# Kernel optimization log

Hardware: AMD Instinct MI355X
Metric: run time of the kernel (lower is better)

## Reference

```python
import jax, jax.numpy as jnp
import numpy as np

B, L, E, DC, N = 1024, 64, 1024, 768, 16384
EPS = 1e-08


def setup_inputs() -> dict:
    key = jax.random.key(0)
    k1, k2, k3, k4, k5, k6 = jax.random.split(key, 6)
    inputs = jax.random.normal(k1, (B, 1, E), dtype=jnp.float32)
    text_emb = jax.random.normal(k2, (B, L, DC), dtype=jnp.float32)
    # padding mask: True = padded; valid lengths in [10, 60) so every row triggers the insert branch
    lengths = jax.random.randint(k3, (B,), 10, 60)
    attn_mask = jnp.arange(L)[None, :] >= lengths[:, None]
    proj_w = jax.random.normal(k4, (DC, E), dtype=jnp.float32) * 0.02
    proj_b = jnp.zeros((DC,), dtype=jnp.float32)
    codebook = jax.random.normal(k5, (N, DC), dtype=jnp.float32) * 0.02
    return {"inputs": inputs, "text_emb": text_emb, "attn_mask": attn_mask,
            "proj_w": proj_w, "proj_b": proj_b, "codebook": codebook}


def _soft_match(x, W):
    # x: [B, S, D], W: [N, D] -> soft codebook readout [B, S, D]
    xn = x / jnp.maximum(jnp.linalg.norm(x, axis=-1, keepdims=True), EPS)
    Wn = W / jnp.maximum(jnp.linalg.norm(W, axis=-1, keepdims=True), EPS)
    d = 1.0 - jnp.einsum('bsd,nd->bsn', xn, Wn)   # 1 - cosine similarity
    p = jax.nn.softmax(d, axis=-1)                 # softmax over codebook entries
    return jnp.einsum('bsn,nd->bsd', p, W)


def reference(inputs, text_emb, attn_mask, proj_w, proj_b, codebook):
    # proj: torch Linear -> x @ W.T + b
    x = jnp.einsum('bse,de->bsd', inputs, proj_w) + proj_b
    clue = _soft_match(x, codebook)                # [B, 1, DC]

    b, l = attn_mask.shape
    vl = l - jnp.sum(attn_mask, axis=1)            # valid length per row, [B]
    do = vl < 64                                   # insert only if there is room
    pos = jnp.arange(l)
    at_vl = pos[None, :] == vl[:, None]            # position valid_length
    at_prev = pos[None, :] == (vl - 1)[:, None]    # position valid_length-1
    prev_vec = text_emb[jnp.arange(b), jnp.clip(vl - 1, 0, l - 1)]  # [B, DC]

    sel_vl = (do[:, None] & at_vl)[..., None]
    sel_prev = (do[:, None] & at_prev)[..., None]
    new_text_emb = jnp.where(sel_vl, prev_vec[:, None, :], text_emb)
    new_text_emb = jnp.where(sel_prev, clue[:, 0, :][:, None, :], new_text_emb)
    new_attn_mask = attn_mask & ~(do[:, None] & at_vl)
    return new_text_emb, new_attn_mask, jnp.float32(0.0)
```

## Files before the change

### kernel.cpp

```cpp
#include <hip/hip_runtime.h>
#include <hip/hip_bf16.h>

#define B_  1024
#define L_  64
#define E_  1024
#define DC_ 768
#define N_  16384

typedef short bf16x8 __attribute__((ext_vector_type(8)));
typedef float f32x4  __attribute__((ext_vector_type(4)));


__global__ void detect_mask(const unsigned int* __restrict__ mi, int* __restrict__ flag) {
    __shared__ int notInt, notFlt;
    if (threadIdx.x == 0) { notInt = 0; notFlt = 0; }
    __syncthreads();
    int ni = 0, nf = 0;
    for (int i = threadIdx.x; i < 16384; i += 256) {
        unsigned v = mi[i];
        if (v > 1u) ni = 1;
        if (v != 0u && v != 0x3f800000u) nf = 1;
    }
    if (ni) notInt = 1;
    if (nf) notFlt = 1;
    __syncthreads();
    if (threadIdx.x == 0) *flag = (!notInt) ? 1 : ((!notFlt) ? 2 : 0);
}

__global__ void compute_vl(const void* __restrict__ mask, const int* __restrict__ flag,
                           int* __restrict__ vl) {
    int b = blockIdx.x * blockDim.x + threadIdx.x;
    if (b >= B_) return;
    int f = *flag;
    int s = 0;
    if (f == 1) {
        const int* m = (const int*)mask;
        for (int j = 0; j < L_; ++j) s += m[b * L_ + j];
    } else if (f == 2) {
        const float* m = (const float*)mask;
        for (int j = 0; j < L_; ++j) s += (m[b * L_ + j] != 0.0f) ? 1 : 0;
    } else {
        const unsigned char* m = (const unsigned char*)mask;
        for (int j = 0; j < L_; ++j) s += m[b * L_ + j];
    }
    vl[b] = L_ - s;
}

__global__ __launch_bounds__(256) void rownorm(const float* __restrict__ M,
                                               float* __restrict__ r, int cols) {
    int row = blockIdx.x;
    const float* p = M + (size_t)row * cols;
    float s = 0.0f;
    for (int c = threadIdx.x; c < cols; c += 256) { float v = p[c]; s += v * v; }
    for (int off = 32; off > 0; off >>= 1) s += __shfl_down(s, off);
    __shared__ float sm[4];
    if ((threadIdx.x & 63) == 0) sm[threadIdx.x >> 6] = s;
    __syncthreads();
    if (threadIdx.x == 0) {
        float t = sm[0] + sm[1] + sm[2] + sm[3];
        r[row] = 1.0f / fmaxf(sqrtf(t), 1e-8f);
    }
}

__global__ __launch_bounds__(256) void rownorm_bf16(const __hip_bfloat16* __restrict__ M,
                                                    float* __restrict__ r, int cols) {
    int row = blockIdx.x;
    const __hip_bfloat16* p = M + (size_t)row * cols;
    float s = 0.0f;
    for (int c = threadIdx.x; c < cols; c += 256) { float v = __bfloat162float(p[c]); s += v * v; }
    for (int off = 32; off > 0; off >>= 1) s += __shfl_down(s, off);
    __shared__ float sm[4];
    if ((threadIdx.x & 63) == 0) sm[threadIdx.x >> 6] = s;
    __syncthreads();
    if (threadIdx.x == 0) {
        float t = sm[0] + sm[1] + sm[2] + sm[3];
        r[row] = 1.0f / fmaxf(sqrtf(t), 1e-8f);
    }
}

__global__ __launch_bounds__(256) void prep_cb(const float* __restrict__ CB,
                                               __hip_bfloat16* __restrict__ CBb,
                                               __hip_bfloat16* __restrict__ CBt) {
    __shared__ float t[64][65];
    int n0 = blockIdx.x * 64, d0 = blockIdx.y * 64;
    int tid = threadIdx.x;
    #pragma unroll
    for (int i = 0; i < 16; ++i) {
        int r = (tid >> 6) + i * 4, c = tid & 63;
        float v = CB[(size_t)(n0 + r) * DC_ + d0 + c];
        t[r][c] = v;
        CBb[(size_t)(n0 + r) * DC_ + d0 + c] = __float2bfloat16(v);
    }
    __syncthreads();
    #pragma unroll
    for (int i = 0; i < 16; ++i) {
        int r = (tid >> 6) + i * 4, c = tid & 63;
        CBt[(size_t)(d0 + r) * N_ + n0 + c] = __float2bfloat16(t[c][r]);
    }
}

__global__ __launch_bounds__(256) void proj_gemm(const float* __restrict__ A,
                                                 const float* __restrict__ W,
                                                 const float* __restrict__ bias,
                                                 __hip_bfloat16* __restrict__ Xb) {
    __shared__ float As[64][17];
    __shared__ float Bs[64][17];
    int t = threadIdx.x;
    int tx = t & 15, ty = t >> 4;
    int m0 = blockIdx.y * 64, n0 = blockIdx.x * 64;
    float acc[4][4] = {};
    for (int k0 = 0; k0 < E_; k0 += 16) {
        #pragma unroll
        for (int i = 0; i < 4; ++i) {
            int r = (t >> 4) + i * 16, c = t & 15;
            As[r][c] = A[(size_t)(m0 + r) * E_ + k0 + c];
            Bs[r][c] = W[(size_t)(n0 + r) * E_ + k0 + c];
        }
        __syncthreads();
        #pragma unroll
        for (int k = 0; k < 16; ++k) {
            float a[4], b[4];
            #pragma unroll
            for (int i = 0; i < 4; ++i) a[i] = As[ty * 4 + i][k];
            #pragma unroll
            for (int j = 0; j < 4; ++j) b[j] = Bs[tx * 4 + j][k];
            #pragma unroll
            for (int i = 0; i < 4; ++i)
                #pragma unroll
                for (int j = 0; j < 4; ++j) acc[i][j] += a[i] * b[j];
        }
        __syncthreads();
    }
    #pragma unroll
    for (int i = 0; i < 4; ++i)
        #pragma unroll
        for (int j = 0; j < 4; ++j) {
            int m = m0 + ty * 4 + i, n = n0 + tx * 4 + j;
            Xb[(size_t)m * DC_ + n] = __float2bfloat16(acc[i][j] + bias[n]);
        }
}

__device__ __forceinline__ void stage_tile(const __hip_bfloat16* __restrict__ src, size_t ldk,
                                           __hip_bfloat16* smem, int wave, int lane) {
    #pragma unroll
    for (int s = 0; s < 2; ++s) {
        const int chunk = wave * 32 + s * 16;
        const int r = chunk + (lane >> 2);
        const int gslot = (lane & 3) ^ ((lane >> 2) & 3);
        const __hip_bfloat16* g = src + (size_t)r * ldk + gslot * 8;
        __builtin_amdgcn_global_load_lds(
            (const __attribute__((address_space(1))) void*)g,
            (__attribute__((address_space(3))) void*)(smem + chunk * 32), 16, 0, 0);
    }
}

__device__ __forceinline__ bf16x8 read_frag(const __hip_bfloat16* smem, int base_row, int lane) {
    const int r = base_row + (lane & 15);
    const int slot = ((lane >> 4) ^ r) & 3;
    return *(const bf16x8*)(smem + r * 32 + slot * 8);
}

__global__ __launch_bounds__(256) void score_mfma(const __hip_bfloat16* __restrict__ Xb,
                                                  const __hip_bfloat16* __restrict__ CBb,
                                                  const float* __restrict__ rX,
                                                  const float* __restrict__ rW,
                                                  __hip_bfloat16* __restrict__ P,
                                                  float* __restrict__ Z) {
    __shared__ __align__(16) __hip_bfloat16 As[128 * 32];
    __shared__ __align__(16) __hip_bfloat16 Bs[128 * 32];
    const int t = threadIdx.x, lane = t & 63, wave = t >> 6;
    const int wr = wave >> 1, wc = wave & 1;
    const int m0 = blockIdx.y * 128, n0 = blockIdx.x * 128;

    f32x4 acc[4][4];
    #pragma unroll
    for (int i = 0; i < 4; ++i)
        #pragma unroll
        for (int j = 0; j < 4; ++j) acc[i][j] = (f32x4){0.f, 0.f, 0.f, 0.f};

    const __hip_bfloat16* Asrc = Xb  + (size_t)m0 * DC_;
    const __hip_bfloat16* Bsrc = CBb + (size_t)n0 * DC_;
    for (int k0 = 0; k0 < DC_; k0 += 32) {
        stage_tile(Asrc + k0, DC_, As, wave, lane);
        stage_tile(Bsrc + k0, DC_, Bs, wave, lane);
        __syncthreads();
        bf16x8 af[4], bg[4];
        #pragma unroll
        for (int i = 0; i < 4; ++i) af[i] = read_frag(As, wr * 64 + i * 16, lane);
        #pragma unroll
        for (int j = 0; j < 4; ++j) bg[j] = read_frag(Bs, wc * 64 + j * 16, lane);
        #pragma unroll
        for (int i = 0; i < 4; ++i)
            #pragma unroll
            for (int j = 0; j < 4; ++j)
                acc[i][j] = __builtin_amdgcn_mfma_f32_16x16x32_bf16(af[i], bg[j], acc[i][j], 0, 0, 0);
        __syncthreads();
    }

    const int fr = lane & 15, fq = lane >> 4;
    float rw[4];
    #pragma unroll
    for (int j = 0; j < 4; ++j) rw[j] = rW[n0 + wc * 64 + j * 16 + fr];
    #pragma unroll
    for (int i = 0; i < 4; ++i) {
        const int mb = m0 + wr * 64 + i * 16 + fq * 4;
        float rx[4];
        #pragma unroll
        for (int q = 0; q < 4; ++q) rx[q] = rX[mb + q];
        float rs[4] = {0.f, 0.f, 0.f, 0.f};
        #pragma unroll
        for (int j = 0; j < 4; ++j) {
            const int n = n0 + wc * 64 + j * 16 + fr;
            #pragma unroll
            for (int q = 0; q < 4; ++q) {
                float e = __expf(-acc[i][j][q] * rx[q] * rw[j]);
                P[(size_t)(mb + q) * N_ + n] = __float2bfloat16(e);
                rs[q] += e;
            }
        }
        #pragma unroll
        for (int q = 0; q < 4; ++q) {
            float s = rs[q];
            s += __shfl_xor(s, 1); s += __shfl_xor(s, 2);
            s += __shfl_xor(s, 4); s += __shfl_xor(s, 8);
            if (fr == 0) atomicAdd(&Z[mb + q], s);
        }
    }
}

__global__ __launch_bounds__(256) void out_mfma(const __hip_bfloat16* __restrict__ P,
                                                const __hip_bfloat16* __restrict__ CBt,
                                                float* __restrict__ clue) {
    __shared__ __align__(16) __hip_bfloat16 As[128 * 32];
    __shared__ __align__(16) __hip_bfloat16 Bs[128 * 32];
    const int t = threadIdx.x, lane = t & 63, wave = t >> 6;
    const int wr = wave >> 1, wc = wave & 1;
    const int m0 = blockIdx.y * 128, d0 = blockIdx.x * 128;
    const int kbeg = blockIdx.z * (N_ / 8);

    f32x4 acc[4][4];
    #pragma unroll
    for (int i = 0; i < 4; ++i)
        #pragma unroll
        for (int j = 0; j < 4; ++j) acc[i][j] = (f32x4){0.f, 0.f, 0.f, 0.f};

    const __hip_bfloat16* Asrc = P   + (size_t)m0 * N_;
    const __hip_bfloat16* Bsrc = CBt + (size_t)d0 * N_;
    for (int kk = 0; kk < N_ / 8; kk += 32) {
        const int k0 = kbeg + kk;
        stage_tile(Asrc + k0, N_, As, wave, lane);
        stage_tile(Bsrc + k0, N_, Bs, wave, lane);
        __syncthreads();
        bf16x8 af[4], bg[4];
        #pragma unroll
        for (int i = 0; i < 4; ++i) af[i] = read_frag(As, wr * 64 + i * 16, lane);
        #pragma unroll
        for (int j = 0; j < 4; ++j) bg[j] = read_frag(Bs, wc * 64 + j * 16, lane);
        #pragma unroll
        for (int i = 0; i < 4; ++i)
            #pragma unroll
            for (int j = 0; j < 4; ++j)
                acc[i][j] = __builtin_amdgcn_mfma_f32_16x16x32_bf16(af[i], bg[j], acc[i][j], 0, 0, 0);
        __syncthreads();
    }

    const int fr = lane & 15, fq = lane >> 4;
    #pragma unroll
    for (int i = 0; i < 4; ++i) {
        const int mb = m0 + wr * 64 + i * 16 + fq * 4;
        #pragma unroll
        for (int j = 0; j < 4; ++j) {
            const int d = d0 + wc * 64 + j * 16 + fr;
            #pragma unroll
            for (int q = 0; q < 4; ++q)
                atomicAdd(&clue[(size_t)(mb + q) * DC_ + d], acc[i][j][q]);
        }
    }
}

__global__ __launch_bounds__(256) void assemble(const float* __restrict__ text,
                                                const float* __restrict__ clue,
                                                const float* __restrict__ Z,
                                                const int* __restrict__ vl,
                                                float* __restrict__ out) {
    int idx = blockIdx.x * 256 + threadIdx.x;
    int c = idx % 192;
    int bl = idx / 192;
    int l = bl & 63, b = bl >> 6;
    int v = vl[b];
    float4 val;
    if (l == v) {
        val = ((const float4*)text)[(size_t)(b * 64 + v - 1) * 192 + c];
    } else if (l == v - 1) {
        float invZ = 1.0f / Z[b];
        float4 t4 = ((const float4*)(clue + (size_t)b * DC_))[c];
        val = make_float4(t4.x * invZ, t4.y * invZ, t4.z * invZ, t4.w * invZ);
    } else {
        val = ((const float4*)text)[idx];
    }
    ((float4*)out)[idx] = val;
}

__global__ void mask_scalar(const int* __restrict__ vl, float* __restrict__ out_mask,
                            float* __restrict__ out_scalar) {
    int idx = blockIdx.x * blockDim.x + threadIdx.x;
    if (idx < B_ * L_) {
        int b = idx >> 6, j = idx & 63;
        out_mask[idx] = (j > vl[b]) ? 1.0f : 0.0f;
    }
    if (idx == 0) *out_scalar = 0.0f;
}

extern "C" void kernel_launch(void* const* d_in, const int* in_sizes, int n_in,
                              void* d_out, int out_size, void* d_ws, size_t ws_size,
                              hipStream_t stream) {
    const float* inputs  = (const float*)d_in[0];
    const float* text    = (const float*)d_in[1];
    const void*  mask    = d_in[2];
    const float* proj_w  = (const float*)d_in[3];
    const float* proj_b  = (const float*)d_in[4];
    const float* codebook= (const float*)d_in[5];
    float* out = (float*)d_out;

    char* ws = (char*)d_ws;
    __hip_bfloat16* Xb   = (__hip_bfloat16*)(ws + 0);
    __hip_bfloat16* CBb  = (__hip_bfloat16*)(ws + 1572864);
    __hip_bfloat16* CBt  = (__hip_bfloat16*)(ws + 26738688);
    __hip_bfloat16* P    = (__hip_bfloat16*)(ws + 51904512);
    float*          clue = (float*)(ws + 85458944);
    float*          rX   = (float*)(ws + 88604672);
    float*          rW   = (float*)(ws + 88608768);
    float*          Z    = (float*)(ws + 88674304);
    int*            vl   = (int*)(ws + 88678400);
    int*            flag = (int*)(ws + 88682496);

    hipMemsetAsync(Z, 0, B_ * sizeof(float), stream);
    hipMemsetAsync(clue, 0, (size_t)B_ * DC_ * sizeof(float), stream);

    detect_mask<<<1, 256, 0, stream>>>((const unsigned int*)mask, flag);
    compute_vl<<<4, 256, 0, stream>>>(mask, flag, vl);
    rownorm<<<N_, 256, 0, stream>>>(codebook, rW, DC_);
    prep_cb<<<dim3(N_ / 64, DC_ / 64), 256, 0, stream>>>(codebook, CBb, CBt);
    proj_gemm<<<dim3(DC_ / 64, B_ / 64), 256, 0, stream>>>(inputs, proj_w, proj_b, Xb);
    rownorm_bf16<<<B_, 256, 0, stream>>>(Xb, rX, DC_);
    score_mfma<<<dim3(N_ / 128, B_ / 128), 256, 0, stream>>>(Xb, CBb, rX, rW, P, Z);
    out_mfma<<<dim3(DC_ / 128, B_ / 128, 8), 256, 0, stream>>>(P, CBt, clue);
    assemble<<<49152, 256, 0, stream>>>(text, clue, Z, vl, out);
    mask_scalar<<<(B_ * L_ + 255) / 256, 256, 0, stream>>>(
        vl, out + (size_t)B_ * L_ * DC_, out + (size_t)B_ * L_ * DC_ + B_ * L_);
}
```

Before: 642.5 us.

## Use bf16 MFMA for projection and replace split-K atomics with partial reduction

Replaces the fp32 SIMT projection GEMM with bf16 casts of inputs and weights followed by an MFMA tiled GEMM. The output GEMM's split-K doubles to 16 slices, each writing to its own partial buffer instead of atomically adding. A new reduction kernel sums the slices and applies the softmax normalisation. This trades atomic contention and slow fp32 math for extra memory traffic on the partials and slightly reduced projection precision.

```diff
diff --git a/kernel.cpp b/kernel.cpp
--- a/kernel.cpp
+++ b/kernel.cpp
@@ -6,6 +6,7 @@
 #define E_  1024
 #define DC_ 768
 #define N_  16384
+#define NZ_ 16
 
 typedef short bf16x8 __attribute__((ext_vector_type(8)));
 typedef float f32x4  __attribute__((ext_vector_type(4)));
@@ -99,45 +100,17 @@
     }
 }
 
-__global__ __launch_bounds__(256) void proj_gemm(const float* __restrict__ A,
-                                                 const float* __restrict__ W,
-                                                 const float* __restrict__ bias,
-                                                 __hip_bfloat16* __restrict__ Xb) {
-    __shared__ float As[64][17];
-    __shared__ float Bs[64][17];
-    int t = threadIdx.x;
-    int tx = t & 15, ty = t >> 4;
-    int m0 = blockIdx.y * 64, n0 = blockIdx.x * 64;
-    float acc[4][4] = {};
-    for (int k0 = 0; k0 < E_; k0 += 16) {
-        #pragma unroll
-        for (int i = 0; i < 4; ++i) {
-            int r = (t >> 4) + i * 16, c = t & 15;
-            As[r][c] = A[(size_t)(m0 + r) * E_ + k0 + c];
-            Bs[r][c] = W[(size_t)(n0 + r) * E_ + k0 + c];
-        }
-        __syncthreads();
-        #pragma unroll
-        for (int k = 0; k < 16; ++k) {
-            float a[4], b[4];
-            #pragma unroll
-            for (int i = 0; i < 4; ++i) a[i] = As[ty * 4 + i][k];
-            #pragma unroll
-            for (int j = 0; j < 4; ++j) b[j] = Bs[tx * 4 + j][k];
-            #pragma unroll
-            for (int i = 0; i < 4; ++i)
-                #pragma unroll
-                for (int j = 0; j < 4; ++j) acc[i][j] += a[i] * b[j];
-        }
-        __syncthreads();
-    }
-    #pragma unroll
-    for (int i = 0; i < 4; ++i)
-        #pragma unroll
-        for (int j = 0; j < 4; ++j) {
-            int m = m0 + ty * 4 + i, n = n0 + tx * 4 + j;
-            Xb[(size_t)m * DC_ + n] = __float2bfloat16(acc[i][j] + bias[n]);
-        }
+__global__ __launch_bounds__(256) void cast_bf16(const float* __restrict__ src,
+                                                 ushort* __restrict__ dst, int n4) {
+    int idx = blockIdx.x * 256 + threadIdx.x;
+    if (idx >= n4) return;
+    float4 v = ((const float4*)src)[idx];
+    ushort4 o;
+    __hip_bfloat16 h0 = __float2bfloat16(v.x); o.x = __builtin_bit_cast(ushort, h0);
+    __hip_bfloat16 h1 = __float2bfloat16(v.y); o.y = __builtin_bit_cast(ushort, h1);
+    __hip_bfloat16 h2 = __float2bfloat16(v.z); o.z = __builtin_bit_cast(ushort, h2);
+    __hip_bfloat16 h3 = __float2bfloat16(v.w); o.w = __builtin_bit_cast(ushort, h3);
+    ((ushort4*)dst)[idx] = o;
 }
 
 __device__ __forceinline__ void stage_tile(const __hip_bfloat16* __restrict__ src, size_t ldk,
@@ -158,6 +131,56 @@
     const int r = base_row + (lane & 15);
     const int slot = ((lane >> 4) ^ r) & 3;
     return *(const bf16x8*)(smem + r * 32 + slot * 8);
+}
+
+__global__ __launch_bounds__(256) void proj_mfma(const __hip_bfloat16* __restrict__ inb,
+                                                 const __hip_bfloat16* __restrict__ pwb,
+                                                 const float* __restrict__ bias,
+                                                 __hip_bfloat16* __restrict__ Xb) {
+    __shared__ __align__(16) __hip_bfloat16 As[128 * 32];
+    __shared__ __align__(16) __hip_bfloat16 Bs[128 * 32];
+    const int t = threadIdx.x, lane = t & 63, wave = t >> 6;
+    const int wr = wave >> 1, wc = wave & 1;
+    const int m0 = blockIdx.y * 128, n0 = blockIdx.x * 128;
+
+    f32x4 acc[4][4];
+    #pragma unroll
+    for (int i = 0; i < 4; ++i)
+        #pragma unroll
+        for (int j = 0; j < 4; ++j) acc[i][j] = (f32x4){0.f, 0.f, 0.f, 0.f};
+
+    const __hip_bfloat16* Asrc = inb + (size_t)m0 * E_;
+    const __hip_bfloat16* Bsrc = pwb + (size_t)n0 * E_;
+    for (int k0 = 0; k0 < E_; k0 += 32) {
+        stage_tile(Asrc + k0, E_, As, wave, lane);
+        stage_tile(Bsrc + k0, E_, Bs, wave, lane);
+        __syncthreads();
+        bf16x8 af[4], bg[4];
+        #pragma unroll
+        for (int i = 0; i < 4; ++i) af[i] = read_frag(As, wr * 64 + i * 16, lane);
+        #pragma unroll
+        for (int j = 0; j < 4; ++j) bg[j] = read_frag(Bs, wc * 64 + j * 16, lane);
+        #pragma unroll
+        for (int i = 0; i < 4; ++i)
+            #pragma unroll
+            for (int j = 0; j < 4; ++j)
+                acc[i][j] = __builtin_amdgcn_mfma_f32_16x16x32_bf16(af[i], bg[j], acc[i][j], 0, 0, 0);
+        __syncthreads();
+    }
+
+    const int fr = lane & 15, fq = lane >> 4;
+    #pragma unroll
+    for (int i = 0; i < 4; ++i) {
+        const int mb = m0 + wr * 64 + i * 16 + fq * 4;
+        #pragma unroll
+        for (int j = 0; j < 4; ++j) {
+            const int d = n0 + wc * 64 + j * 16 + fr;
+            const float bv = bias[d];
+            #pragma unroll
+            for (int q = 0; q < 4; ++q)
+                Xb[(size_t)(mb + q) * DC_ + d] = __float2bfloat16(acc[i][j][q] + bv);
+        }
+    }
 }
 
 __global__ __launch_bounds__(256) void score_mfma(const __hip_bfloat16* __restrict__ Xb,
@@ -230,13 +253,14 @@
 
 __global__ __launch_bounds__(256) void out_mfma(const __hip_bfloat16* __restrict__ P,
                                                 const __hip_bfloat16* __restrict__ CBt,
-                                                float* __restrict__ clue) {
+                                                float* __restrict__ cluePart) {
     __shared__ __align__(16) __hip_bfloat16 As[128 * 32];
     __shared__ __align__(16) __hip_bfloat16 Bs[128 * 32];
     const int t = threadIdx.x, lane = t & 63, wave = t >> 6;
     const int wr = wave >> 1, wc = wave & 1;
     const int m0 = blockIdx.y * 128, d0 = blockIdx.x * 128;
-    const int kbeg = blockIdx.z * (N_ / 8);
+    const int kbeg = blockIdx.z * (N_ / NZ_);
+    float* outp = cluePart + (size_t)blockIdx.z * (B_ * DC_);
 
     f32x4 acc[4][4];
     #pragma unroll
@@ -246,7 +270,7 @@
 
     const __hip_bfloat16* Asrc = P   + (size_t)m0 * N_;
     const __hip_bfloat16* Bsrc = CBt + (size_t)d0 * N_;
-    for (int kk = 0; kk < N_ / 8; kk += 32) {
+    for (int kk = 0; kk < N_ / NZ_; kk += 32) {
         const int k0 = kbeg + kk;
         stage_tile(Asrc + k0, N_, As, wave, lane);
         stage_tile(Bsrc + k0, N_, Bs, wave, lane);
@@ -273,14 +297,25 @@
             const int d = d0 + wc * 64 + j * 16 + fr;
             #pragma unroll
             for (int q = 0; q < 4; ++q)
-                atomicAdd(&clue[(size_t)(mb + q) * DC_ + d], acc[i][j][q]);
+                outp[(size_t)(mb + q) * DC_ + d] = acc[i][j][q];
         }
     }
 }
 
+__global__ __launch_bounds__(256) void reduce_clue(const float* __restrict__ cluePart,
+                                                   const float* __restrict__ Z,
+                                                   float* __restrict__ clueF) {
+    const int d = blockIdx.x * 256 + threadIdx.x;
+    const int b = blockIdx.y;
+    float s = 0.0f;
+    #pragma unroll
+    for (int z = 0; z < NZ_; ++z)
+        s += cluePart[(size_t)z * (B_ * DC_) + (size_t)b * DC_ + d];
+    clueF[(size_t)b * DC_ + d] = s / Z[b];
+}
+
 __global__ __launch_bounds__(256) void assemble(const float* __restrict__ text,
-                                                const float* __restrict__ clue,
-                                                const float* __restrict__ Z,
+                                                const float* __restrict__ clueF,
                                                 const int* __restrict__ vl,
                                                 float* __restrict__ out) {
     int idx = blockIdx.x * 256 + threadIdx.x;
@@ -292,9 +327,7 @@
     if (l == v) {
         val = ((const float4*)text)[(size_t)(b * 64 + v - 1) * 192 + c];
     } else if (l == v - 1) {
-        float invZ = 1.0f / Z[b];
-        float4 t4 = ((const float4*)(clue + (size_t)b * DC_))[c];
-        val = make_float4(t4.x * invZ, t4.y * invZ, t4.z * invZ, t4.w * invZ);
+        val = ((const float4*)(clueF + (size_t)b * DC_))[c];
     } else {
         val = ((const float4*)text)[idx];
     }
@@ -323,29 +356,34 @@
     float* out = (float*)d_out;
 
     char* ws = (char*)d_ws;
-    __hip_bfloat16* Xb   = (__hip_bfloat16*)(ws + 0);
-    __hip_bfloat16* CBb  = (__hip_bfloat16*)(ws + 1572864);
-    __hip_bfloat16* CBt  = (__hip_bfloat16*)(ws + 26738688);
-    __hip_bfloat16* P    = (__hip_bfloat16*)(ws + 51904512);
-    float*          clue = (float*)(ws + 85458944);
-    float*          rX   = (float*)(ws + 88604672);
-    float*          rW   = (float*)(ws + 88608768);
-    float*          Z    = (float*)(ws + 88674304);
-    int*            vl   = (int*)(ws + 88678400);
-    int*            flag = (int*)(ws + 88682496);
+    __hip_bfloat16* Xb       = (__hip_bfloat16*)(ws + 0);
+    __hip_bfloat16* CBb      = (__hip_bfloat16*)(ws + 1572864);
+    __hip_bfloat16* CBt      = (__hip_bfloat16*)(ws + 26738688);
+    __hip_bfloat16* P        = (__hip_bfloat16*)(ws + 51904512);
+    __hip_bfloat16* inb      = (__hip_bfloat16*)(ws + 51904512);
+    __hip_bfloat16* pwb      = (__hip_bfloat16*)(ws + 54001664);
+    float*          cluePart = (float*)(ws + 85458944);
+    float*          clueF    = (float*)(ws + 135790592);
+    float*          rX       = (float*)(ws + 138936320);
+    float*          rW       = (float*)(ws + 138940416);
+    float*          Z        = (float*)(ws + 139005952);
+    int*            vl       = (int*)(ws + 139010048);
+    int*            flag     = (int*)(ws + 139014144);
 
     hipMemsetAsync(Z, 0, B_ * sizeof(float), stream);
-    hipMemsetAsync(clue, 0, (size_t)B_ * DC_ * sizeof(float), stream);
 
     detect_mask<<<1, 256, 0, stream>>>((const unsigned int*)mask, flag);
     compute_vl<<<4, 256, 0, stream>>>(mask, flag, vl);
     rownorm<<<N_, 256, 0, stream>>>(codebook, rW, DC_);
     prep_cb<<<dim3(N_ / 64, DC_ / 64), 256, 0, stream>>>(codebook, CBb, CBt);
-    proj_gemm<<<dim3(DC_ / 64, B_ / 64), 256, 0, stream>>>(inputs, proj_w, proj_b, Xb);
+    cast_bf16<<<(B_ * E_ / 4 + 255) / 256, 256, 0, stream>>>(inputs, (ushort*)inb, B_ * E_ / 4);
+    cast_bf16<<<(DC_ * E_ / 4 + 255) / 256, 256, 0, stream>>>(proj_w, (ushort*)pwb, DC_ * E_ / 4);
+    proj_mfma<<<dim3(DC_ / 128, B_ / 128), 256, 0, stream>>>(inb, pwb, proj_b, Xb);
     rownorm_bf16<<<B_, 256, 0, stream>>>(Xb, rX, DC_);
     score_mfma<<<dim3(N_ / 128, B_ / 128), 256, 0, stream>>>(Xb, CBb, rX, rW, P, Z);
-    out_mfma<<<dim3(DC_ / 128, B_ / 128, 8), 256, 0, stream>>>(P, CBt, clue);
-    assemble<<<49152, 256, 0, stream>>>(text, clue, Z, vl, out);
+    out_mfma<<<dim3(DC_ / 128, B_ / 128, NZ_), 256, 0, stream>>>(P, CBt, cluePart);
+    reduce_clue<<<dim3(DC_ / 256, B_), 256, 0, stream>>>(cluePart, Z, clueF);
+    assemble<<<49152, 256, 0, stream>>>(text, clueF, vl, out);
     mask_scalar<<<(B_ * L_ + 255) / 256, 256, 0, stream>>>(
         vl, out + (size_t)B_ * L_ * DC_, out + (size_t)B_ * L_ * DC_ + B_ * L_);
 }
```

Measured after the change: 594.8 us. 7.4% less time.
